# Kernel optimization log

Hardware: AMD Instinct MI355X
Metric: run time of the kernel (lower is better)

Reference implementation:

```python
import jax, jax.numpy as jnp
import numpy as np

B, S, D, H, DFF, NB = 32, 512, 512, 8, 2048, 2
DK = D // H
L = 2 * NB
NEG = -1e32


def setup_inputs():
    key = jax.random.key(0)
    ks = jax.random.split(key, 8)
    sc = 1.0 / np.sqrt(D)
    return {
        "q_embed_data": jax.random.normal(ks[0], (B, S, D), jnp.float32),
        "qa_embed_data": jax.random.normal(ks[1], (B, S, D), jnp.float32),
        "Wk": jax.random.normal(ks[2], (L, D, D), jnp.float32) * sc,
        "bk": jnp.zeros((L, D), jnp.float32),
        "Wv": jax.random.normal(ks[3], (L, D, D), jnp.float32) * sc,
        "bv": jnp.zeros((L, D), jnp.float32),
        "Wo": jax.random.normal(ks[4], (L, D, D), jnp.float32) * sc,
        "bo": jnp.zeros((L, D), jnp.float32),
        "gammas": jax.random.normal(ks[5], (L, H), jnp.float32) * 0.5,
        "ln1_g": jnp.ones((L, D), jnp.float32),
        "ln1_b": jnp.zeros((L, D), jnp.float32),
        "W1": jax.random.normal(ks[6], (L, DFF, D), jnp.float32) * sc,
        "b1": jnp.zeros((L, DFF), jnp.float32),
        "W2": jax.random.normal(ks[7], (L, D, DFF), jnp.float32) * (1.0 / np.sqrt(DFF)),
        "b2": jnp.zeros((L, D), jnp.float32),
        "ln2_g": jnp.ones((L, D), jnp.float32),
        "ln2_b": jnp.zeros((L, D), jnp.float32),
    }


def _layer_norm(x, g, b):
    mu = jnp.mean(x, -1, keepdims=True)
    var = jnp.mean((x - mu) ** 2, -1, keepdims=True)
    return (x - mu) / jnp.sqrt(var + 1e-5) * g + b


def _mha(xq, xk, xv, Wk, bk, Wv, bv, Wo, bo, gam, mask, zero_pad):
    # torch Linear: x @ W.T + b; kq_same=1 -> q uses k_linear
    def proj(x, W, b):
        return (x @ W.T + b).reshape(B, S, H, DK).transpose(0, 2, 1, 3)

    q, k, v = proj(xq, Wk, bk), proj(xk, Wk, bk), proj(xv, Wv, bv)
    scores = jnp.einsum('bhid,bhjd->bhij', q, k) / np.sqrt(DK)  # [B,H,S,S]
    # monotonic distance-decay (no-grad in original)
    sm = jax.nn.softmax(jnp.where(mask, scores, NEG), -1) * mask
    sm = jax.lax.stop_gradient(sm)
    distcum = jnp.cumsum(sm, -1)
    disttot = jnp.sum(sm, -1, keepdims=True)
    idx = jnp.arange(S)
    pos = jnp.abs(idx[None, :] - idx[:, None]).astype(jnp.float32)  # |j - i|
    dist = jax.lax.stop_gradient(
        jnp.sqrt(jnp.clip((disttot - distcum) * pos, 0.0, None)))
    g = -jax.nn.softplus(gam)[None, :, None, None]  # [1,H,1,1]
    te = jnp.clip(jnp.exp(dist * g), 1e-5, 1e5)
    attn = jax.nn.softmax(jnp.where(mask, scores * te, NEG), -1)
    if zero_pad:
        attn = attn.at[:, :, 0, :].set(0.0)
    out = jnp.einsum('bhij,bhjd->bhid', attn, v)
    out = out.transpose(0, 2, 1, 3).reshape(B, S, D)
    return out @ Wo.T + bo


def _forward(q_embed_data, qa_embed_data, Wk, bk, Wv, bv, Wo, bo, gammas,
             ln1_g, ln1_b, W1, b1, W2, b2, ln2_g, ln2_b):
    idx = jnp.arange(S)
    mask0 = idx[None, :] < idx[:, None]    # triu(k=0)==0: strictly past only
    mask1 = idx[None, :] <= idx[:, None]   # triu(k=1)==0: causal incl. diag
    x, y = q_embed_data, qa_embed_data
    for l in range(L):
        first = (l % 2 == 0)
        vals = y if first else x
        mask = mask0 if first else mask1
        q2 = _mha(x, x, vals, Wk[l], bk[l], Wv[l], bv[l], Wo[l], bo[l],
                  gammas[l], mask, zero_pad=first)
        x = _layer_norm(x + q2, ln1_g[l], ln1_b[l])
        if first:  # apply_pos=True only on the mask=0 layers
            ffn = jax.nn.relu(x @ W1[l].T + b1[l]) @ W2[l].T + b2[l]
            x = _layer_norm(x + ffn, ln2_g[l], ln2_b[l])
    return x


def reference(q_embed_data, qa_embed_data, Wk, bk, Wv, bv, Wo, bo, gammas,
              ln1_g, ln1_b, W1, b1, W2, b2, ln2_g, ln2_b):
    return _forward(q_embed_data, qa_embed_data, Wk, bk, Wv, bv, Wo, bo,
                    gammas, ln1_g, ln1_b, W1, b1, W2, b2, ln2_g, ln2_b)
```

## Files before the change

kernel.cpp:

```cpp
#include <hip/hip_runtime.h>
#include <hip/hip_bf16.h>
#include <math.h>

#define B_ 32
#define S_ 512
#define D_ 512
#define H_ 8
#define DK_ 64
#define DFF_ 2048
#define L_ 4

typedef __attribute__((ext_vector_type(8))) short bf16x8;
typedef __attribute__((ext_vector_type(4))) float f32x4;

__device__ __forceinline__ unsigned short f2bf(float x) {
  union { float f; unsigned u; } v; v.f = x;
  unsigned r = v.u + 0x7fff + ((v.u >> 16) & 1);
  return (unsigned short)(r >> 16);
}

__device__ __forceinline__ unsigned short f2h(float x) {
  union { _Float16 h; unsigned short u; } v;
  v.h = (_Float16)x;
  return v.u;
}
__device__ __forceinline__ float h2f(unsigned short u) {
  union { _Float16 h; unsigned short u; } v;
  v.u = u;
  return (float)v.h;
}

__device__ __forceinline__ void load_lds16(const void* g, void* l) {
  __builtin_amdgcn_global_load_lds(
      (const __attribute__((address_space(1))) void*)g,
      (__attribute__((address_space(3))) void*)l, 16, 0, 0);
}

__global__ __launch_bounds__(256) void cvt_f32_bf16(
    const float* __restrict__ in, unsigned short* __restrict__ out, size_t n8)
{
  size_t idx = (size_t)blockIdx.x * 256 + threadIdx.x;
  size_t stride = (size_t)gridDim.x * 256;
  for (size_t i = idx; i < n8; i += stride) {
    const float4* p = (const float4*)(in + i * 8);
    float4 a = p[0], b = p[1];
    union { unsigned short u[8]; int4 v; } o;
    o.u[0] = f2bf(a.x); o.u[1] = f2bf(a.y); o.u[2] = f2bf(a.z); o.u[3] = f2bf(a.w);
    o.u[4] = f2bf(b.x); o.u[5] = f2bf(b.y); o.u[6] = f2bf(b.z); o.u[7] = f2bf(b.w);
    *(int4*)(out + i * 8) = o.v;
  }
}

__global__ __launch_bounds__(256) void copy_cvt(
    const float* __restrict__ in, float* __restrict__ outf,
    unsigned short* __restrict__ outb, size_t n8)
{
  size_t idx = (size_t)blockIdx.x * 256 + threadIdx.x;
  size_t stride = (size_t)gridDim.x * 256;
  for (size_t i = idx; i < n8; i += stride) {
    const float4* p = (const float4*)(in + i * 8);
    float4 a = p[0], b = p[1];
    ((float4*)(outf + i * 8))[0] = a;
    ((float4*)(outf + i * 8))[1] = b;
    union { unsigned short u[8]; int4 v; } o;
    o.u[0] = f2bf(a.x); o.u[1] = f2bf(a.y); o.u[2] = f2bf(a.z); o.u[3] = f2bf(a.w);
    o.u[4] = f2bf(b.x); o.u[5] = f2bf(b.y); o.u[6] = f2bf(b.z); o.u[7] = f2bf(b.w);
    *(int4*)(outb + i * 8) = o.v;
  }
}

__global__ __launch_bounds__(256) void gemm_bt_bf16(
    const unsigned short* __restrict__ A, const unsigned short* __restrict__ W,
    const float* __restrict__ bias,
    float* __restrict__ Cf, unsigned short* __restrict__ Cb,
    int M, int N, int K, int relu)
{
  __shared__ __align__(16) short As[128 * 32];
  __shared__ __align__(16) short Ws[128 * 32];
  int tid = threadIdx.x;
  int lane = tid & 63, w = tid >> 6;
  int wr = w >> 1, wc = w & 1;
  int bm = blockIdx.y * 128, bn = blockIdx.x * 128;

  f32x4 acc[4][4];
  #pragma unroll
  for (int m = 0; m < 4; ++m)
    #pragma unroll
    for (int n = 0; n < 4; ++n) acc[m][n] = (f32x4){0.f, 0.f, 0.f, 0.f};

  int srow = tid >> 2;
  int skB  = (tid & 3) * 16;
  const char* pa0 = (const char*)(A + (size_t)(bm + srow) * K) + skB;
  const char* pa1 = (const char*)(A + (size_t)(bm + 64 + srow) * K) + skB;
  const char* pw0 = (const char*)(W + (size_t)(bn + srow) * K) + skB;
  const char* pw1 = (const char*)(W + (size_t)(bn + 64 + srow) * K) + skB;
  char* lA0 = (char*)As + w * 1024;
  char* lA1 = (char*)As + 4096 + w * 1024;
  char* lW0 = (char*)Ws + w * 1024;
  char* lW1 = (char*)Ws + 4096 + w * 1024;

  int r = lane & 15, k8 = lane >> 4;
  const bf16x8* Arow = (const bf16x8*)As;
  const bf16x8* Wrow = (const bf16x8*)Ws;

  for (int k0 = 0; k0 < K; k0 += 32) {
    load_lds16(pa0, lA0);
    load_lds16(pa1, lA1);
    load_lds16(pw0, lW0);
    load_lds16(pw1, lW1);
    pa0 += 64; pa1 += 64; pw0 += 64; pw1 += 64;
    __syncthreads();
    bf16x8 aF[4], bF[4];
    #pragma unroll
    for (int m = 0; m < 4; ++m) aF[m] = Arow[(wr * 64 + m * 16 + r) * 4 + k8];
    #pragma unroll
    for (int n = 0; n < 4; ++n) bF[n] = Wrow[(wc * 64 + n * 16 + r) * 4 + k8];
    #pragma unroll
    for (int m = 0; m < 4; ++m)
      #pragma unroll
      for (int n = 0; n < 4; ++n)
        acc[m][n] = __builtin_amdgcn_mfma_f32_16x16x32_bf16(aF[m], bF[n], acc[m][n], 0, 0, 0);
    __syncthreads();
  }

  int orow0 = bm + wr * 64 + (lane >> 4) * 4;
  int ocol0 = bn + wc * 64 + (lane & 15);
  #pragma unroll
  for (int n = 0; n < 4; ++n) {
    int col = ocol0 + n * 16;
    float bv = bias[col];
    #pragma unroll
    for (int m = 0; m < 4; ++m) {
      int row = orow0 + m * 16;
      #pragma unroll
      for (int j = 0; j < 4; ++j) {
        float val = acc[m][n][j] + bv;
        if (relu) val = fmaxf(val, 0.f);
        size_t off = (size_t)(row + j) * N + col;
        if (Cf) Cf[off] = val; else Cb[off] = f2bf(val);
      }
    }
  }
}

__global__ __launch_bounds__(256) void transpose_heads_bf16(
    const unsigned short* __restrict__ v, unsigned short* __restrict__ vt)
{
  __shared__ unsigned short t[64][65];
  int jt = blockIdx.x, h = blockIdx.y, b = blockIdx.z;
  int lane = threadIdx.x & 63, w = threadIdx.x >> 6;
  #pragma unroll
  for (int r = 0; r < 16; ++r) {
    int j = w + r * 4;
    t[j][lane] = v[((size_t)(b * S_ + jt * 64 + j)) * D_ + h * DK_ + lane];
  }
  __syncthreads();
  #pragma unroll
  for (int r = 0; r < 16; ++r) {
    int d = w + r * 4;
    vt[((size_t)((b * H_ + h) * DK_ + d)) * S_ + jt * 64 + lane] = t[lane][d];
  }
}

__device__ __forceinline__ f32x4 qk_tile(
    int kt, int qt, int i0, int g, int c15, int maskType,
    const unsigned short* kbase, bf16x8 aQ0, bf16x8 aQ1)
{
  const unsigned short* kr = kbase + (size_t)(kt * 16 + c15) * D_;
  bf16x8 bK0 = *(const bf16x8*)(kr);
  bf16x8 bK1 = *(const bf16x8*)(kr + 32);
  f32x4 c = (f32x4){0.f, 0.f, 0.f, 0.f};
  c = __builtin_amdgcn_mfma_f32_16x16x32_bf16(aQ0, bK0, c, 0, 0, 0);
  c = __builtin_amdgcn_mfma_f32_16x16x32_bf16(aQ1, bK1, c, 0, 0, 0);
  #pragma unroll
  for (int r = 0; r < 4; ++r) c[r] *= 0.125f;
  if (kt == qt) {
    int j = kt * 16 + c15;
    #pragma unroll
    for (int r = 0; r < 4; ++r) {
      int i = i0 + 4 * g + r;
      bool valid = maskType ? (j <= i) : (j < i);
      if (!valid) c[r] = -1e30f;
    }
  }
  return c;
}

__global__ __launch_bounds__(128) void attn_mfma3(
    const unsigned short* __restrict__ qkb,
    const unsigned short* __restrict__ vtb,
    const float* __restrict__ gammas,
    unsigned short* __restrict__ ao,
    int maskType)
{
  __shared__ __align__(16) unsigned short scr_all[33 * 16][16];
  __shared__ __align__(16) unsigned short P_all[2][16][48];
  int tid = threadIdx.x;
  int lane = tid & 63, w = tid >> 6;
  int bid = blockIdx.x;
  int p = bid & 15;
  int h = (bid >> 4) & (H_ - 1);
  int b = bid >> 7;
  int qt = w ? (31 - p) : p;
  int rowbase = w ? (p + 1) * 16 : 0;
  unsigned short (*scr)[16] = &scr_all[rowbase];
  unsigned short (*P_lds)[48] = P_all[w];
  int i0 = qt * 16;
  int c15 = lane & 15, g = lane >> 4;

  const unsigned short* qbase =
      qkb + ((size_t)(b * S_ + i0 + c15)) * D_ + h * DK_ + g * 8;
  bf16x8 aQ0 = *(const bf16x8*)(qbase);
  bf16x8 aQ1 = *(const bf16x8*)(qbase + 32);
  const unsigned short* kbase = qkb + ((size_t)b * S_) * D_ + h * DK_ + g * 8;

  float gam = gammas[h];
  float gneg = -((gam > 20.f) ? gam : log1pf(__expf(gam)));

  float m1[4] = {-1e30f, -1e30f, -1e30f, -1e30f};
  for (int kt = 0; kt <= qt; ++kt) {
    f32x4 c = qk_tile(kt, qt, i0, g, c15, maskType, kbase, aQ0, aQ1);
    int j = kt * 16 + c15;
    int lo = (int)f2h(c[0]) | ((int)f2h(c[1]) << 16);
    int hi = (int)f2h(c[2]) | ((int)f2h(c[3]) << 16);
    *(int2*)&scr[j][4 * g] = make_int2(lo, hi);
    #pragma unroll
    for (int r = 0; r < 4; ++r) m1[r] = fmaxf(m1[r], c[r]);
  }
  #pragma unroll
  for (int r = 0; r < 4; ++r)
    #pragma unroll
    for (int off = 1; off < 16; off <<= 1)
      m1[r] = fmaxf(m1[r], __shfl_xor(m1[r], off, 64));
  asm volatile("s_waitcnt lgkmcnt(0)" ::: "memory");
  __builtin_amdgcn_sched_barrier(0);

  float sum1[4] = {0.f, 0.f, 0.f, 0.f};
  for (int kt = 0; kt <= qt; ++kt) {
    int j = kt * 16 + c15;
    int2 d = *(const int2*)&scr[j][4 * g];
    float s0 = h2f((unsigned short)(d.x & 0xffff));
    float s1 = h2f((unsigned short)((unsigned)d.x >> 16));
    float s2_ = h2f((unsigned short)(d.y & 0xffff));
    float s3 = h2f((unsigned short)((unsigned)d.y >> 16));
    sum1[0] += __expf(s0 - m1[0]);
    sum1[1] += __expf(s1 - m1[1]);
    sum1[2] += __expf(s2_ - m1[2]);
    sum1[3] += __expf(s3 - m1[3]);
  }
  #pragma unroll
  for (int r = 0; r < 4; ++r)
    #pragma unroll
    for (int off = 1; off < 16; off <<= 1)
      sum1[r] += __shfl_xor(sum1[r], off, 64);
  float inv1[4], m2b[4];
  #pragma unroll
  for (int r = 0; r < 4; ++r) {
    inv1[r] = (sum1[r] > 0.f) ? 1.f / sum1[r] : 0.f;
    m2b[r] = fmaxf(m1[r], 0.f);
  }

  f32x4 acc[4];
  #pragma unroll
  for (int dt = 0; dt < 4; ++dt) acc[dt] = (f32x4){0.f, 0.f, 0.f, 0.f};
  float sum2[4] = {0.f, 0.f, 0.f, 0.f};
  {
    float carry[4] = {0.f, 0.f, 0.f, 0.f};
    const unsigned short* vbase =
        vtb + (((size_t)(b * H_ + h) * DK_) + c15) * S_ + g * 8;

    #pragma unroll
    for (int jc = 0; jc < 16; ++jc) {
      if (jc * 2 <= qt) {
        #pragma unroll
        for (int t2 = 0; t2 < 2; ++t2) {
          int kt = jc * 2 + t2;
          if (kt <= qt) {
            int j = kt * 16 + c15;
            int2 d = *(const int2*)&scr[j][4 * g];
            float sv[4];
            sv[0] = h2f((unsigned short)(d.x & 0xffff));
            sv[1] = h2f((unsigned short)((unsigned)d.x >> 16));
            sv[2] = h2f((unsigned short)(d.y & 0xffff));
            sv[3] = h2f((unsigned short)((unsigned)d.y >> 16));
            #pragma unroll
            for (int r = 0; r < 4; ++r) {
              float e = __expf(sv[r] - m1[r]);
              float p2 = e;
              #pragma unroll
              for (int off = 1; off < 16; off <<= 1) {
                float t = __shfl_up(p2, off, 16);
                if (c15 >= off) p2 += t;
              }
              float tot = __shfl(p2, lane | 15, 64);
              float cum = carry[r] + p2;
              carry[r] += tot;
              float suffix = sum1[r] - cum;
              int i = i0 + 4 * g + r;
              float pos = fabsf((float)(kt * 16 + c15 - i));
              float dist = sqrtf(fmaxf(suffix * inv1[r] * pos, 0.f));
              float te = fminf(fmaxf(__expf(dist * gneg), 1e-5f), 1e5f);
              float s2 = sv[r] * te;
              float e2 = __expf(s2 - m2b[r]);
              sum2[r] += e2;
              P_lds[4 * g + r][t2 * 16 + c15] = f2bf(e2);
            }
          } else {
            #pragma unroll
            for (int r = 0; r < 4; ++r) P_lds[4 * g + r][t2 * 16 + c15] = 0;
          }
        }
        asm volatile("s_waitcnt lgkmcnt(0)" ::: "memory");
        __builtin_amdgcn_sched_barrier(0);
        bf16x8 aP = *(const bf16x8*)&P_lds[c15][g * 8];
        const unsigned short* vr = vbase + (size_t)jc * 32;
        #pragma unroll
        for (int dt = 0; dt < 4; ++dt) {
          bf16x8 bV = *(const bf16x8*)(vr + (size_t)dt * 16 * S_);
          acc[dt] = __builtin_amdgcn_mfma_f32_16x16x32_bf16(aP, bV, acc[dt], 0, 0, 0);
        }
        asm volatile("s_waitcnt lgkmcnt(0)" ::: "memory");
        __builtin_amdgcn_sched_barrier(0);
      }
    }
  }
  #pragma unroll
  for (int r = 0; r < 4; ++r)
    #pragma unroll
    for (int off = 1; off < 16; off <<= 1)
      sum2[r] += __shfl_xor(sum2[r], off, 64);

  int zp = (maskType == 0 && qt == 0);
  #pragma unroll
  for (int dt = 0; dt < 4; ++dt) {
    #pragma unroll
    for (int r = 0; r < 4; ++r) {
      int i = i0 + 4 * g + r;
      float ns = (sum2[r] > 0.f) ? 1.f / sum2[r] : 0.f;
      float val = acc[dt][r] * ns;
      if (zp && (4 * g + r) == 0) val = 0.f;
      ao[((size_t)(b * S_ + i)) * D_ + h * DK_ + dt * 16 + c15] = f2bf(val);
    }
  }
}

__device__ __forceinline__ float blockReduceSum256(float v, float* red) {
  #pragma unroll
  for (int off = 32; off > 0; off >>= 1) v += __shfl_down(v, off, 64);
  int lane = threadIdx.x & 63, wid = threadIdx.x >> 6;
  __syncthreads();
  if (lane == 0) red[wid] = v;
  __syncthreads();
  return red[0] + red[1] + red[2] + red[3];
}

__global__ __launch_bounds__(256) void add_ln(
    float* __restrict__ x, unsigned short* __restrict__ xb,
    const float* __restrict__ r,
    const float* __restrict__ g, const float* __restrict__ b)
{
  int row = blockIdx.x;
  int t = threadIdx.x;
  float* xr = x + (size_t)row * D_;
  unsigned short* xbr = xb + (size_t)row * D_;
  const float* rr = r + (size_t)row * D_;
  float v0 = xr[t] + rr[t];
  float v1 = xr[t + 256] + rr[t + 256];
  __shared__ float red[4];
  float s = blockReduceSum256(v0 + v1, red);
  float mu = s * (1.0f / 512.0f);
  float d0 = v0 - mu, d1 = v1 - mu;
  float sq = blockReduceSum256(d0 * d0 + d1 * d1, red);
  float rstd = rsqrtf(sq * (1.0f / 512.0f) + 1e-5f);
  float o0 = d0 * rstd * g[t] + b[t];
  float o1 = d1 * rstd * g[t + 256] + b[t + 256];
  xr[t] = o0;
  xr[t + 256] = o1;
  xbr[t] = f2bf(o0);
  xbr[t + 256] = f2bf(o1);
}

static inline void cvt(const float* in, unsigned short* out, size_t n, hipStream_t s) {
  size_t n8 = n / 8;
  int blocks = (int)((n8 + 255) / 256);
  if (blocks > 2048) blocks = 2048;
  cvt_f32_bf16<<<blocks, 256, 0, s>>>(in, out, n8);
}

extern "C" void kernel_launch(void* const* d_in, const int* in_sizes, int n_in,
                              void* d_out, int out_size, void* d_ws, size_t ws_size,
                              hipStream_t stream) {
  const float* q_embed  = (const float*)d_in[0];
  const float* qa_embed = (const float*)d_in[1];
  const float* Wk = (const float*)d_in[2];
  const float* bk = (const float*)d_in[3];
  const float* Wv = (const float*)d_in[4];
  const float* bv = (const float*)d_in[5];
  const float* Wo = (const float*)d_in[6];
  const float* bo = (const float*)d_in[7];
  const float* gammas = (const float*)d_in[8];
  const float* ln1_g = (const float*)d_in[9];
  const float* ln1_b = (const float*)d_in[10];
  const float* W1 = (const float*)d_in[11];
  const float* b1 = (const float*)d_in[12];
  const float* W2 = (const float*)d_in[13];
  const float* b2 = (const float*)d_in[14];
  const float* ln2_g = (const float*)d_in[15];
  const float* ln2_b = (const float*)d_in[16];

  float* x = (float*)d_out;
  const size_t NTOK = (size_t)B_ * S_;
  const size_t ND = NTOK * D_;

  float* qkf = (float*)d_ws;
  unsigned short* xb    = (unsigned short*)(qkf + ND);
  unsigned short* valsb = xb + ND;
  unsigned short* qkb   = valsb + ND;
  unsigned short* vb    = qkb + ND;
  unsigned short* vtb   = vb + ND;
  unsigned short* aob   = vtb + ND;
  unsigned short* wkb   = aob + ND;
  unsigned short* wvb   = wkb + (size_t)L_ * D_ * D_;
  unsigned short* wob   = wvb + (size_t)L_ * D_ * D_;
  unsigned short* w1b   = wob + (size_t)L_ * D_ * D_;
  unsigned short* w2b   = w1b + (size_t)L_ * DFF_ * D_;
  unsigned short* ffnb  = qkb;

  {
    size_t n8 = ND / 8;
    copy_cvt<<<2048, 256, 0, stream>>>(q_embed, x, xb, n8);
  }

  cvt(Wk, wkb, (size_t)L_ * D_ * D_, stream);
  cvt(Wv, wvb, (size_t)L_ * D_ * D_, stream);
  cvt(Wo, wob, (size_t)L_ * D_ * D_, stream);
  cvt(W1, w1b, (size_t)L_ * DFF_ * D_, stream);
  cvt(W2, w2b, (size_t)L_ * DFF_ * D_, stream);
  cvt(qa_embed, valsb, ND, stream);

  dim3 gproj(D_ / 128, NTOK / 128);
  dim3 gf1(DFF_ / 128, NTOK / 128);
  dim3 gf2(D_ / 128, NTOK / 128);
  dim3 gtr(S_ / 64, H_, B_);
  int gattn = B_ * H_ * 16;

  for (int l = 0; l < L_; ++l) {
    int first = (l % 2 == 0);
    const unsigned short* vA = first ? valsb : xb;

    gemm_bt_bf16<<<gproj, 256, 0, stream>>>(xb, wkb + (size_t)l * D_ * D_, bk + l * D_,
                                            nullptr, qkb, (int)NTOK, D_, D_, 0);
    gemm_bt_bf16<<<gproj, 256, 0, stream>>>(vA, wvb + (size_t)l * D_ * D_, bv + l * D_,
                                            nullptr, vb, (int)NTOK, D_, D_, 0);
    transpose_heads_bf16<<<gtr, 256, 0, stream>>>(vb, vtb);
    attn_mfma3<<<gattn, 128, 0, stream>>>(qkb, vtb, gammas + l * H_, aob, first ? 0 : 1);
    gemm_bt_bf16<<<gproj, 256, 0, stream>>>(aob, wob + (size_t)l * D_ * D_, bo + l * D_,
                                            qkf, nullptr, (int)NTOK, D_, D_, 0);
    add_ln<<<(int)NTOK, 256, 0, stream>>>(x, xb, qkf, ln1_g + l * D_, ln1_b + l * D_);
    if (first) {
      gemm_bt_bf16<<<gf1, 256, 0, stream>>>(xb, w1b + (size_t)l * DFF_ * D_, b1 + l * DFF_,
                                            nullptr, ffnb, (int)NTOK, DFF_, D_, 1);
      gemm_bt_bf16<<<gf2, 256, 0, stream>>>(ffnb, w2b + (size_t)l * D_ * DFF_, b2 + l * D_,
                                            qkf, nullptr, (int)NTOK, D_, DFF_, 0);
      add_ln<<<(int)NTOK, 256, 0, stream>>>(x, xb, qkf, ln2_g + l * D_, ln2_b + l * D_);
    }
  }
}
```

Before: 1.210 ms.

## Use DPP row scan for cumulative softmax and pack two wave-pairs per block

The 16-lane inclusive prefix sum in the distance-decay loop, previously built from shuffles, now uses DPP row_shr adds, and the row total is broadcast with ds_swizzle. The attention kernel also grows from 128 to 256 threads, so each block handles two balanced query-tile pairs, with the LDS score and P buffers duplicated per pair and the grid halved. The aim is fewer cross-lane instructions in the hot inner loop and fewer, larger blocks. The risks are the higher LDS use per block, which can limit occupancy, and the correctness of the DPP bound_ctrl zero-fill and the swizzle broadcast pattern.

```diff
diff --git a/kernel.cpp b/kernel.cpp
--- a/kernel.cpp
+++ b/kernel.cpp
@@ -28,6 +28,23 @@
   union { _Float16 h; unsigned short u; } v;
   v.u = u;
   return (float)v.h;
+}
+
+#define DPP_ADD_SHR(x, N)                                                       \
+  {                                                                             \
+    int _t = __builtin_amdgcn_update_dpp(0, __float_as_int(x), 0x110 + (N),     \
+                                         0xf, 0xf, true);                       \
+    (x) += __int_as_float(_t);                                                  \
+  }
+__device__ __forceinline__ float scan16_dpp(float x) {
+  DPP_ADD_SHR(x, 1);
+  DPP_ADD_SHR(x, 2);
+  DPP_ADD_SHR(x, 4);
+  DPP_ADD_SHR(x, 8);
+  return x;
+}
+__device__ __forceinline__ float bcast15(float x) {
+  return __int_as_float(__builtin_amdgcn_ds_swizzle(__float_as_int(x), 0x1FF));
 }
 
 __device__ __forceinline__ void load_lds16(const void* g, void* l) {
@@ -186,24 +203,26 @@
   return c;
 }
 
-__global__ __launch_bounds__(128) void attn_mfma3(
+__global__ __launch_bounds__(256) void attn_mfma3(
     const unsigned short* __restrict__ qkb,
     const unsigned short* __restrict__ vtb,
     const float* __restrict__ gammas,
     unsigned short* __restrict__ ao,
     int maskType)
 {
-  __shared__ __align__(16) unsigned short scr_all[33 * 16][16];
-  __shared__ __align__(16) unsigned short P_all[2][16][48];
+  __shared__ __align__(16) unsigned short scr_all[2][33 * 16][16];
+  __shared__ __align__(16) unsigned short P_all[4][16][48];
   int tid = threadIdx.x;
   int lane = tid & 63, w = tid >> 6;
   int bid = blockIdx.x;
-  int p = bid & 15;
-  int h = (bid >> 4) & (H_ - 1);
-  int b = bid >> 7;
-  int qt = w ? (31 - p) : p;
-  int rowbase = w ? (p + 1) * 16 : 0;
-  unsigned short (*scr)[16] = &scr_all[rowbase];
+  int pp = bid & 7;
+  int h = (bid >> 3) & (H_ - 1);
+  int b = bid >> 6;
+  int pairIdx = w >> 1, wp = w & 1;
+  int p = pp * 2 + pairIdx;
+  int qt = wp ? (31 - p) : p;
+  int rowbase = wp ? (p + 1) * 16 : 0;
+  unsigned short (*scr)[16] = &scr_all[pairIdx][rowbase];
   unsigned short (*P_lds)[48] = P_all[w];
   int i0 = qt * 16;
   int c15 = lane & 15, g = lane >> 4;
@@ -286,13 +305,8 @@
             #pragma unroll
             for (int r = 0; r < 4; ++r) {
               float e = __expf(sv[r] - m1[r]);
-              float p2 = e;
-              #pragma unroll
-              for (int off = 1; off < 16; off <<= 1) {
-                float t = __shfl_up(p2, off, 16);
-                if (c15 >= off) p2 += t;
-              }
-              float tot = __shfl(p2, lane | 15, 64);
+              float p2 = scan16_dpp(e);
+              float tot = bcast15(p2);
               float cum = carry[r] + p2;
               carry[r] += tot;
               float suffix = sum1[r] - cum;
@@ -442,7 +456,7 @@
   dim3 gf1(DFF_ / 128, NTOK / 128);
   dim3 gf2(D_ / 128, NTOK / 128);
   dim3 gtr(S_ / 64, H_, B_);
-  int gattn = B_ * H_ * 16;
+  int gattn = B_ * H_ * 8;
 
   for (int l = 0; l < L_; ++l) {
     int first = (l % 2 == 0);
@@ -453,7 +467,7 @@
     gemm_bt_bf16<<<gproj, 256, 0, stream>>>(vA, wvb + (size_t)l * D_ * D_, bv + l * D_,
                                             nullptr, vb, (int)NTOK, D_, D_, 0);
     transpose_heads_bf16<<<gtr, 256, 0, stream>>>(vb, vtb);
-    attn_mfma3<<<gattn, 128, 0, stream>>>(qkb, vtb, gammas + l * H_, aob, first ? 0 : 1);
+    attn_mfma3<<<gattn, 256, 0, stream>>>(qkb, vtb, gammas + l * H_, aob, first ? 0 : 1);
     gemm_bt_bf16<<<gproj, 256, 0, stream>>>(aob, wob + (size_t)l * D_ * D_, bo + l * D_,
                                             qkf, nullptr, (int)NTOK, D_, D_, 0);
     add_ln<<<(int)NTOK, 256, 0, stream>>>(x, xb, qkf, ln1_g + l * D_, ln1_b + l * D_);
```

Measured after the change: 1.184 ms. 1.02x faster.
